# Optimization experiments

Measured on AMD Instinct MI355X. Metric: run time of the kernel, lower is better.

Reference implementation:

```python
import jax, jax.numpy as jnp
import numpy as np

D_MODEL = 1024
N_HEADS = 16
HEAD_DIM = D_MODEL // N_HEADS
N_SCALES = 11
_D4 = jnp.array([0.4829629131445341, 0.8365163037378079, 0.2241438680420134, -0.1294095225512604], dtype=jnp.float32)


def setup_inputs() -> dict:
    key = jax.random.key(0)
    ks = jax.random.split(key, 8)
    B, N, D = 8, 2048, D_MODEL
    s = 1.0 / np.sqrt(D)
    x = jax.random.normal(ks[0], (B, N, D), dtype=jnp.float32)
    qkv_w = jax.random.normal(ks[1], (3 * D, D), dtype=jnp.float32) * s
    qkv_b = jnp.zeros((3 * D,), dtype=jnp.float32)
    out_w = jax.random.normal(ks[2], (D, D), dtype=jnp.float32) * s
    out_b = jnp.zeros((D,), dtype=jnp.float32)
    gate_w = jax.random.normal(ks[3], (D, D), dtype=jnp.float32) * s
    gate_b = jnp.full((D,), 2.0, dtype=jnp.float32)  # nn.init.constant_(gate_proj.bias, 2.0)
    scale_gain = jax.random.normal(ks[4], (N_SCALES, N_HEADS), dtype=jnp.float32) * 0.1
    field_coupling = jnp.eye(N_HEADS, dtype=jnp.float32) + 0.01 * jax.random.normal(ks[5], (N_HEADS, N_HEADS), dtype=jnp.float32)
    return {"x": x, "qkv_w": qkv_w, "qkv_b": qkv_b, "out_w": out_w, "out_b": out_b,
            "gate_w": gate_w, "gate_b": gate_b, "scale_gain": scale_gain,
            "field_coupling": field_coupling}


def _causal_multiscale(x_c, scale_gain):
    # x_c: [B, C, N] with channel order (head-major, then head_dim)
    B, C, N = x_c.shape
    gains = jax.nn.softmax(scale_gain, axis=0)              # [S, H]
    gains_exp = jnp.repeat(gains, HEAD_DIM, axis=1)         # [S, C]
    out = jnp.zeros_like(x_c)
    for j in range(N_SCALES):
        d = 1 << j
        xp = jnp.pad(x_c, ((0, 0), (0, 0), (3 * d, 0)))     # causal left pad
        # depthwise dilated conv (cross-correlation, same D4 taps per channel)
        y = (_D4[0] * xp[:, :, 0 * d:0 * d + N]
             + _D4[1] * xp[:, :, 1 * d:1 * d + N]
             + _D4[2] * xp[:, :, 2 * d:2 * d + N]
             + _D4[3] * xp[:, :, 3 * d:3 * d + N])
        out = out + gains_exp[j][None, :, None] * y
    return out


def reference(x, qkv_w, qkv_b, out_w, out_b, gate_w, gate_b, scale_gain, field_coupling):
    B, N, D = x.shape
    H, HD = N_HEADS, HEAD_DIM
    qkv = x @ qkv_w.T + qkv_b                               # [B, N, 3D]
    q, k, v = jnp.split(qkv, 3, axis=-1)                    # q is unused (as in source)
    k = k.reshape(B, N, H, HD)
    v = v.reshape(B, N, H, HD)
    k_mag = jnp.linalg.norm(k, axis=-1, keepdims=True)      # [B, N, H, 1]
    field = v * k_mag                                       # [B, N, H, HD]
    # -> [B, C, N], C = H*HD, head-major channel layout
    x_c = jnp.transpose(field, (0, 2, 3, 1)).reshape(B, H * HD, N)
    out_c = _causal_multiscale(x_c, scale_gain)             # [B, C, N]
    field = out_c.reshape(B, H, HD, N)                      # [B, H, HD, N]
    coupling = jax.nn.softmax(field_coupling, axis=-1)      # [H, H]
    field = jnp.einsum('ij,bjdn->bidn', coupling, field)    # head coupling
    gathered = jnp.transpose(field, (0, 3, 1, 2)).reshape(B, N, D)
    gate = jax.nn.sigmoid(x @ gate_w.T + gate_b)
    return (gathered * gate) @ out_w.T + out_b
```

## Files before the change

kernel.cpp:

```cpp
#include <hip/hip_runtime.h>
#include <hip/hip_bf16.h>
#include <math.h>

#define BD 8
#define SN 2048
#define DM 1024
#define NH 16
#define HD 64
#define NS 11
#define NTAP 24
#define PAD 3072

typedef __attribute__((ext_vector_type(8))) short short8;
typedef __attribute__((ext_vector_type(4))) float floatx4;

constexpr int OFFS[NTAP] = {0, 1, 2, 3, 4, 6, 8, 12, 16, 24, 32, 48, 64, 96,
                            128, 192, 256, 384, 512, 768, 1024, 1536, 2048, 3072};

__device__ __forceinline__ void async_load16(const void* g, void* lds) {
    __builtin_amdgcn_global_load_lds(
        (const __attribute__((address_space(1))) void*)g,
        (__attribute__((address_space(3))) void*)lds,
        16, 0, 0);
}

__device__ __forceinline__ float bf2f(int v) {
    union { unsigned u; float f; } cv;
    cv.u = ((unsigned)v & 0xffffu) << 16;
    return cv.f;
}

__device__ __forceinline__ unsigned short f2bfbits(float x) {
    union { __hip_bfloat16 h; unsigned short u; } cv;
    cv.h = __float2bfloat16(x);
    return cv.u;
}

__global__ __launch_bounds__(256) void f2bf_kernel(const float* __restrict__ src,
                                                   __hip_bfloat16* __restrict__ dst,
                                                   int n4) {
    int i = blockIdx.x * 256 + threadIdx.x;
    if (i < n4) {
        const float4 v = reinterpret_cast<const float4*>(src)[i];
        union { __hip_bfloat16 h[4]; uint2 u; } cv;
        cv.h[0] = __float2bfloat16(v.x);
        cv.h[1] = __float2bfloat16(v.y);
        cv.h[2] = __float2bfloat16(v.z);
        cv.h[3] = __float2bfloat16(v.w);
        reinterpret_cast<uint2*>(dst)[i] = cv.u;
    }
}

__global__ void prep_kernel(const float* __restrict__ scale_gain,
                            const float* __restrict__ field_coupling,
                            const float* __restrict__ qkv_b,
                            const float* __restrict__ gate_b,
                            float* __restrict__ wtab,
                            float* __restrict__ cw,
                            float* __restrict__ biascat)
{
    const float D4[4] = {0.4829629131445341f, 0.8365163037378079f,
                         0.2241438680420134f, -0.1294095225512604f};
    int t = threadIdx.x;
    if (t < NH) {
        float g[NS];
        float m = -1e30f;
        for (int j = 0; j < NS; ++j) m = fmaxf(m, scale_gain[j * NH + t]);
        float s = 0.f;
        for (int j = 0; j < NS; ++j) { g[j] = expf(scale_gain[j * NH + t] - m); s += g[j]; }
        float inv = 1.f / s;
        for (int j = 0; j < NS; ++j) g[j] *= inv;
        for (int i = 0; i < NTAP; ++i) {
            float w = 0.f;
            for (int j = 0; j < NS; ++j)
                for (int tt = 0; tt < 4; ++tt)
                    if (((3 - tt) << j) == OFFS[i]) w += g[j] * D4[tt];
            wtab[i * NH + t] = w;
        }
    } else if (t < 2 * NH) {
        int r = t - NH;
        float m = -1e30f;
        for (int j = 0; j < NH; ++j) m = fmaxf(m, field_coupling[r * NH + j]);
        float e[NH]; float s = 0.f;
        for (int j = 0; j < NH; ++j) { e[j] = expf(field_coupling[r * NH + j] - m); s += e[j]; }
        float inv = 1.f / s;
        for (int j = 0; j < NH; ++j) cw[r * NH + j] = e[j] * inv;
    }
    for (int i = t; i < 2048; i += 256)
        biascat[i] = (i < 1024) ? qkv_b[1024 + i] : gate_b[i - 1024];
}

__global__ __launch_bounds__(256, 3) void gemm128_kernel(
    const __hip_bfloat16* __restrict__ A,
    const __hip_bfloat16* __restrict__ Bw,
    void* __restrict__ Cout,
    const float* __restrict__ bias,
    float* __restrict__ kmag,
    int M, int Nn, int K, int mode) {
    __shared__ short As[128 * 64];
    __shared__ short Bs[128 * 64];

    const int tid = threadIdx.x;
    const int m0 = blockIdx.y * 128;
    const int n0 = blockIdx.x * 128;
    const int wv = tid >> 6;
    const int ln = tid & 63;

    const int srow = ln >> 3;
    const int scc  = (ln & 7) ^ srow;
    size_t goffA[4], goffB[4];
    #pragma unroll
    for (int i = 0; i < 4; ++i) {
        const int row = wv * 32 + i * 8 + srow;
        goffA[i] = (size_t)(m0 + row) * K + scc * 8;
        goffB[i] = (size_t)(n0 + row) * K + scc * 8;
    }

    const int lrow = ln & 15, quad = ln >> 4;
    const int wm = (wv >> 1) * 64;
    const int wn = (wv & 1) * 64;
    int aaddr[4], baddr[4];
    #pragma unroll
    for (int t = 0; t < 4; ++t) {
        const int sw = (quad ^ (lrow & 7)) * 16;
        aaddr[t] = (wm + t * 16 + lrow) * 128 + sw;
        baddr[t] = (wn + t * 16 + lrow) * 128 + sw;
    }

    floatx4 acc[4][4];
    #pragma unroll
    for (int a = 0; a < 4; ++a)
        #pragma unroll
        for (int b = 0; b < 4; ++b) acc[a][b] = (floatx4){0.f, 0.f, 0.f, 0.f};

    for (int kt = 0; kt < K; kt += 64) {
        #pragma unroll
        for (int i = 0; i < 4; ++i) {
            async_load16(A + goffA[i] + kt, &As[(wv * 32 + i * 8) * 64]);
            async_load16(Bw + goffB[i] + kt, &Bs[(wv * 32 + i * 8) * 64]);
        }
        __syncthreads();
        #pragma unroll
        for (int h = 0; h < 2; ++h) {
            short8 a[4], b[4];
            #pragma unroll
            for (int t = 0; t < 4; ++t) {
                a[t] = *reinterpret_cast<const short8*>(
                           reinterpret_cast<const char*>(As) + (aaddr[t] ^ (h * 64)));
                b[t] = *reinterpret_cast<const short8*>(
                           reinterpret_cast<const char*>(Bs) + (baddr[t] ^ (h * 64)));
            }
            #pragma unroll
            for (int mt = 0; mt < 4; ++mt)
                #pragma unroll
                for (int nt = 0; nt < 4; ++nt)
                    acc[mt][nt] = __builtin_amdgcn_mfma_f32_16x16x32_bf16(
                        a[mt], b[nt], acc[mt][nt], 0, 0, 0);
        }
        __syncthreads();
    }

    if (mode == 2 && n0 < 1024) {
        const int h = (n0 + wn) >> 6;
        #pragma unroll
        for (int mt = 0; mt < 4; ++mt) {
            #pragma unroll
            for (int i = 0; i < 4; ++i) {
                float ss = 0.f;
                #pragma unroll
                for (int nt = 0; nt < 4; ++nt) {
                    const float v = acc[mt][nt][i] + bias[n0 + wn + nt * 16 + lrow];
                    ss += v * v;
                }
                ss += __shfl_xor(ss, 1);
                ss += __shfl_xor(ss, 2);
                ss += __shfl_xor(ss, 4);
                ss += __shfl_xor(ss, 8);
                if (lrow == 0) {
                    const int r = m0 + wm + mt * 16 + quad * 4 + i;
                    kmag[h * (BD * SN) + r] = sqrtf(ss);
                }
            }
        }
        return;
    }

    #pragma unroll
    for (int mt = 0; mt < 4; ++mt) {
        #pragma unroll
        for (int nt = 0; nt < 4; ++nt) {
            const int col = n0 + wn + nt * 16 + lrow;
            float bv = 0.f;
            if (bias && mode != 1) bv = bias[col];
            #pragma unroll
            for (int i = 0; i < 4; ++i) {
                const int row = m0 + wm + mt * 16 + quad * 4 + i;
                float val = acc[mt][nt][i] + bv;
                if (mode == 1 && bias) val += bias[row];
                if (mode == 0) {
                    ((float*)Cout)[(size_t)row * Nn + col] = val;
                } else if (mode == 1) {
                    ((__hip_bfloat16*)Cout)[(size_t)row * Nn + col] = __float2bfloat16(val);
                } else {
                    val = 1.f / (1.f + expf(-val));
                    ((__hip_bfloat16*)Cout)[(size_t)row * 1024 + (col - 1024)] =
                        __float2bfloat16(val);
                }
            }
        }
    }
}

__global__ __launch_bounds__(256) void wavelet_kernel(const __hip_bfloat16* __restrict__ fieldv,
                                                      const float* __restrict__ kmag,
                                                      const float* __restrict__ wtab,
                                                      __hip_bfloat16* __restrict__ wave) {
    const int bc = blockIdx.x;
    const int b = bc >> 10;
    const int c = bc & (DM - 1);
    const int h = c >> 6;
    __shared__ float row[PAD + SN];
    const int t = threadIdx.x;

    float w[NTAP];
    #pragma unroll
    for (int i = 0; i < NTAP; ++i) w[i] = wtab[i * NH + h];

    {
        float4* r4 = reinterpret_cast<float4*>(row);
        const float4 zv = {0.f, 0.f, 0.f, 0.f};
        #pragma unroll
        for (int i = 0; i < 3; ++i) r4[t + i * 256] = zv;
    }
    {
        const __hip_bfloat16* src = fieldv + (size_t)c * (BD * SN) + b * SN;
        const float* mag = kmag + (size_t)h * (BD * SN) + b * SN;
        const int i = t * 8;
        const short8 s = *reinterpret_cast<const short8*>(src + i);
        const float4 m0 = *reinterpret_cast<const float4*>(mag + i);
        const float4 m1 = *reinterpret_cast<const float4*>(mag + i + 4);
        float4 o0, o1;
        o0.x = bf2f(s[0]) * m0.x; o0.y = bf2f(s[1]) * m0.y;
        o0.z = bf2f(s[2]) * m0.z; o0.w = bf2f(s[3]) * m0.w;
        o1.x = bf2f(s[4]) * m1.x; o1.y = bf2f(s[5]) * m1.y;
        o1.z = bf2f(s[6]) * m1.z; o1.w = bf2f(s[7]) * m1.w;
        *reinterpret_cast<float4*>(&row[PAD + i]) = o0;
        *reinterpret_cast<float4*>(&row[PAD + i + 4]) = o1;
    }
    __syncthreads();

    __hip_bfloat16* dst = wave + (size_t)bc * SN;
    #pragma unroll
    for (int pass = 0; pass < 2; ++pass) {
        const int n = (pass * 256 + t) * 4;
        const float* bp = &row[PAD + n];
        const float4 qc = *reinterpret_cast<const float4*>(bp);
        const float4 qb = *reinterpret_cast<const float4*>(bp - 4);
        const float4 qa = *reinterpret_cast<const float4*>(bp - 8);
        float a0, a1, a2, a3;
        a0 = w[0] * qc.x; a1 = w[0] * qc.y; a2 = w[0] * qc.z; a3 = w[0] * qc.w;
        a0 += w[1] * qb.w; a1 += w[1] * qc.x; a2 += w[1] * qc.y; a3 += w[1] * qc.z;
        a0 += w[2] * qb.z; a1 += w[2] * qb.w; a2 += w[2] * qc.x; a3 += w[2] * qc.y;
        a0 += w[3] * qb.y; a1 += w[3] * qb.z; a2 += w[3] * qb.w; a3 += w[3] * qc.x;
        a0 += w[4] * qb.x; a1 += w[4] * qb.y; a2 += w[4] * qb.z; a3 += w[4] * qb.w;
        a0 += w[5] * qa.z; a1 += w[5] * qa.w; a2 += w[5] * qb.x; a3 += w[5] * qb.y;
        a0 += w[6] * qa.x; a1 += w[6] * qa.y; a2 += w[6] * qa.z; a3 += w[6] * qa.w;
        #pragma unroll
        for (int i = 7; i < NTAP; ++i) {
            const float4 q = *reinterpret_cast<const float4*>(bp - OFFS[i]);
            a0 += w[i] * q.x; a1 += w[i] * q.y; a2 += w[i] * q.z; a3 += w[i] * q.w;
        }
        union { __hip_bfloat16 hh[4]; uint2 u; } cv;
        cv.hh[0] = __float2bfloat16(a0); cv.hh[1] = __float2bfloat16(a1);
        cv.hh[2] = __float2bfloat16(a2); cv.hh[3] = __float2bfloat16(a3);
        *reinterpret_cast<uint2*>(dst + n) = cv.u;
    }
}

__global__ __launch_bounds__(256) void couplegate_kernel(
        const __hip_bfloat16* __restrict__ wave,
        const float* __restrict__ cw,
        const __hip_bfloat16* __restrict__ gate,
        __hip_bfloat16* __restrict__ Ag) {
    const int b = blockIdx.y;
    const int n0 = blockIdx.x * 32;
    __shared__ unsigned short U[33 * 1024];
    __shared__ float cwl[NH * NH];
    const int t = threadIdx.x;
    const int wv = t >> 6, ln = t & 63;

    #pragma unroll
    for (int p = 0; p < 16; ++p) {
        const int u = p * 256 + wv * 64 + ln;
        const int cch = u >> 2, qs = u & 3;
        const int qg = qs ^ (cch & 3);
        async_load16(wave + (size_t)(b * DM + cch) * SN + n0 + qg * 8,
                     (char*)U + (size_t)(p * 256 + wv * 64) * 16);
    }
    cwl[t] = cw[t];
    __syncthreads();

    const int nq = t & 7;
    const int d0 = t >> 3;
    const int d1 = 32 + d0;
    float v0[16][4], v1[16][4];
    #pragma unroll
    for (int hi = 0; hi < 16; ++hi) {
        #pragma unroll
        for (int q = 0; q < 4; ++q) {
            const int s0 = q ^ (d0 & 3);
            const int s1 = q ^ (d1 & 3);
            v0[hi][q] = bf2f(U[(hi * 64 + d0) * 32 + s0 * 8 + nq]);
            v1[hi][q] = bf2f(U[(hi * 64 + d1) * 32 + s1 * 8 + nq]);
        }
    }
    __syncthreads();

    #pragma unroll
    for (int ho = 0; ho < 16; ++ho) {
        float cwr[16];
        #pragma unroll
        for (int j = 0; j < 4; ++j) {
            const float4 c4 = *reinterpret_cast<const float4*>(&cwl[ho * 16 + j * 4]);
            cwr[j * 4 + 0] = c4.x; cwr[j * 4 + 1] = c4.y;
            cwr[j * 4 + 2] = c4.z; cwr[j * 4 + 3] = c4.w;
        }
        float a0[4] = {0.f, 0.f, 0.f, 0.f}, a1[4] = {0.f, 0.f, 0.f, 0.f};
        #pragma unroll
        for (int hi = 0; hi < 16; ++hi) {
            #pragma unroll
            for (int q = 0; q < 4; ++q) {
                a0[q] += cwr[hi] * v0[hi][q];
                a1[q] += cwr[hi] * v1[hi][q];
            }
        }
        #pragma unroll
        for (int q = 0; q < 4; ++q) {
            const int nloc = q * 8 + nq;
            U[nloc * 1032 + ho * 64 + d0] = f2bfbits(a0[q]);
            U[nloc * 1032 + ho * 64 + d1] = f2bfbits(a1[q]);
        }
    }
    __syncthreads();

    #pragma unroll
    for (int p = 0; p < 16; ++p) {
        const int idx = p * 256 + t;
        const int nloc = idx >> 7, cu = idx & 127;
        const short8 ov = *reinterpret_cast<const short8*>(&U[nloc * 1032 + cu * 8]);
        const size_t off = ((size_t)(b * SN + n0 + nloc)) * DM + cu * 8;
        const short8 gv = *reinterpret_cast<const short8*>(
            reinterpret_cast<const unsigned short*>(gate) + off);
        union { __hip_bfloat16 hh[8]; short8 s; } cv;
        #pragma unroll
        for (int j = 0; j < 8; ++j)
            cv.hh[j] = __float2bfloat16(bf2f(ov[j]) * bf2f(gv[j]));
        *reinterpret_cast<short8*>(reinterpret_cast<unsigned short*>(Ag) + off) = cv.s;
    }
}

extern "C" void kernel_launch(void* const* d_in, const int* in_sizes, int n_in,
                              void* d_out, int out_size, void* d_ws, size_t ws_size,
                              hipStream_t stream) {
    const float* x     = (const float*)d_in[0];
    const float* qkv_w = (const float*)d_in[1];
    const float* qkv_b = (const float*)d_in[2];
    const float* out_w = (const float*)d_in[3];
    const float* out_b = (const float*)d_in[4];
    const float* gate_w = (const float*)d_in[5];
    const float* gate_b = (const float*)d_in[6];
    const float* scale_gain = (const float*)d_in[7];
    const float* field_coupling = (const float*)d_in[8];

    char* ws = (char*)d_ws;
    const int M = BD * SN;

    __hip_bfloat16* x_bf    = (__hip_bfloat16*)(ws);
    __hip_bfloat16* wkg_bf  = (__hip_bfloat16*)(ws + 33554432);
    __hip_bfloat16* wv_bf   = (__hip_bfloat16*)(ws + 37748736);
    __hip_bfloat16* wo_bf   = (__hip_bfloat16*)(ws + 39845888);
    float* wtab             = (float*)(ws + 41943040);
    float* cwbuf            = (float*)(ws + 41944576);
    float* biascat          = (float*)(ws + 41945600);
    float* kmag             = (float*)(ws + 41953792);
    __hip_bfloat16* fieldv  = (__hip_bfloat16*)(ws + 43002368);
    __hip_bfloat16* gate_bf = (__hip_bfloat16*)(ws + 76556800);
    __hip_bfloat16* wave_bf = (__hip_bfloat16*)(ws + 110111232);
    __hip_bfloat16* Ag = x_bf;
    float* out = (float*)d_out;

    f2bf_kernel<<<(M * DM / 4 + 255) / 256, 256, 0, stream>>>(x, x_bf, M * DM / 4);
    f2bf_kernel<<<(DM * DM / 4 + 255) / 256, 256, 0, stream>>>(qkv_w + (size_t)DM * DM, wkg_bf, DM * DM / 4);
    f2bf_kernel<<<(DM * DM / 4 + 255) / 256, 256, 0, stream>>>(gate_w, wkg_bf + (size_t)DM * DM, DM * DM / 4);
    f2bf_kernel<<<(DM * DM / 4 + 255) / 256, 256, 0, stream>>>(qkv_w + (size_t)2 * DM * DM, wv_bf, DM * DM / 4);
    f2bf_kernel<<<(DM * DM / 4 + 255) / 256, 256, 0, stream>>>(out_w, wo_bf, DM * DM / 4);

    prep_kernel<<<1, 256, 0, stream>>>(scale_gain, field_coupling, qkv_b, gate_b,
                                       wtab, cwbuf, biascat);

    {
        dim3 grid(2 * DM / 128, M / 128);
        gemm128_kernel<<<grid, 256, 0, stream>>>(x_bf, wkg_bf, gate_bf, biascat, kmag,
                                                 M, 2 * DM, DM, 2);
    }
    {
        dim3 grid(M / 128, DM / 128);
        gemm128_kernel<<<grid, 256, 0, stream>>>(wv_bf, x_bf, fieldv, qkv_b + 2 * DM, nullptr,
                                                 DM, M, DM, 1);
    }
    wavelet_kernel<<<BD * DM, 256, 0, stream>>>(fieldv, kmag, wtab, wave_bf);
    {
        dim3 grid(SN / 32, BD);
        couplegate_kernel<<<grid, 256, 0, stream>>>(wave_bf, cwbuf, gate_bf, Ag);
    }
    {
        dim3 grid(DM / 128, M / 128);
        gemm128_kernel<<<grid, 256, 0, stream>>>(Ag, wo_bf, out, out_b, nullptr,
                                                 M, DM, DM, 0);
    }
}
```

Before: 400.0 us.

## Replace 128x128 GEMM with 256x256 tile, 8-wave, double-buffered pipelined kernel

```diff
diff --git a/kernel.cpp b/kernel.cpp
--- a/kernel.cpp
+++ b/kernel.cpp
@@ -90,86 +90,170 @@
         biascat[i] = (i < 1024) ? qkv_b[1024 + i] : gate_b[i - 1024];
 }
 
-__global__ __launch_bounds__(256, 3) void gemm128_kernel(
+
+#define PHASE_SYNC() do { \
+    __builtin_amdgcn_sched_barrier(0); \
+    __builtin_amdgcn_s_barrier(); \
+    asm volatile("s_waitcnt lgkmcnt(0)" ::: "memory"); \
+    __builtin_amdgcn_sched_barrier(0); \
+} while (0)
+
+#define PHASE_END() do { \
+    __builtin_amdgcn_sched_barrier(0); \
+    __builtin_amdgcn_s_barrier(); \
+} while (0)
+
+#define STAGE(GP, H, KT, LB) do { \
+    _Pragma("unroll") \
+    for (int jj = 0; jj < 2; ++jj) { \
+        const int grow_ = (H) * 128 + jj * 64 + srow; \
+        async_load16((GP) + (size_t)grow_ * K + (KT) + gk8, \
+                     &S[(LB) + ((H) * 128 + jj * 64 + wid8) * 64]); \
+    } \
+} while (0)
+
+#define READ_A(AV, P, MF0) do { \
+    _Pragma("unroll") \
+    for (int mm = 0; mm < 4; ++mm) { \
+        const int off_ = (P) * 32768 + abase + ((MF0) + mm) * 1024; \
+        AV[mm][0] = *reinterpret_cast<const short8*>(&S[off_ + sw0]); \
+        AV[mm][1] = *reinterpret_cast<const short8*>(&S[off_ + sw1]); \
+    } \
+} while (0)
+
+#define READ_B(P, NF0) do { \
+    _Pragma("unroll") \
+    for (int nn = 0; nn < 2; ++nn) { \
+        const int off_ = (P) * 32768 + bbase + ((NF0) + nn) * 1024; \
+        bfr[nn][0] = *reinterpret_cast<const short8*>(&S[off_ + sw0]); \
+        bfr[nn][1] = *reinterpret_cast<const short8*>(&S[off_ + sw1]); \
+    } \
+} while (0)
+
+#define MFMA_Q(AV, MF0, NF0) do { \
+    __builtin_amdgcn_s_setprio(1); \
+    _Pragma("unroll") \
+    for (int mm = 0; mm < 4; ++mm) \
+        _Pragma("unroll") \
+        for (int nn = 0; nn < 2; ++nn) \
+            _Pragma("unroll") \
+            for (int hh = 0; hh < 2; ++hh) \
+                acc[(MF0) + mm][(NF0) + nn] = __builtin_amdgcn_mfma_f32_16x16x32_bf16( \
+                    AV[mm][hh], bfr[nn][hh], acc[(MF0) + mm][(NF0) + nn], 0, 0, 0); \
+    __builtin_amdgcn_s_setprio(0); \
+} while (0)
+
+__global__ __launch_bounds__(512, 2) void gemm256_kernel(
     const __hip_bfloat16* __restrict__ A,
     const __hip_bfloat16* __restrict__ Bw,
     void* __restrict__ Cout,
     const float* __restrict__ bias,
     float* __restrict__ kmag,
     int M, int Nn, int K, int mode) {
-    __shared__ short As[128 * 64];
-    __shared__ short Bs[128 * 64];
+    __shared__ short S[65536];
 
     const int tid = threadIdx.x;
-    const int m0 = blockIdx.y * 128;
-    const int n0 = blockIdx.x * 128;
-    const int wv = tid >> 6;
-    const int ln = tid & 63;
-
-    const int srow = ln >> 3;
-    const int scc  = (ln & 7) ^ srow;
-    size_t goffA[4], goffB[4];
-    #pragma unroll
-    for (int i = 0; i < 4; ++i) {
-        const int row = wv * 32 + i * 8 + srow;
-        goffA[i] = (size_t)(m0 + row) * K + scc * 8;
-        goffB[i] = (size_t)(n0 + row) * K + scc * 8;
-    }
+    const int wid = tid >> 6;
+    const int ln  = tid & 63;
+    const int m0 = blockIdx.y * 256;
+    const int n0 = blockIdx.x * 256;
+
+    const int srow = tid >> 3;
+    const int gk8  = ((tid & 7) ^ (srow & 7)) * 8;
+    const int wid8 = wid * 8;
 
     const int lrow = ln & 15, quad = ln >> 4;
-    const int wm = (wv >> 1) * 64;
-    const int wn = (wv & 1) * 64;
-    int aaddr[4], baddr[4];
-    #pragma unroll
-    for (int t = 0; t < 4; ++t) {
-        const int sw = (quad ^ (lrow & 7)) * 16;
-        aaddr[t] = (wm + t * 16 + lrow) * 128 + sw;
-        baddr[t] = (wn + t * 16 + lrow) * 128 + sw;
-    }
-
-    floatx4 acc[4][4];
-    #pragma unroll
-    for (int a = 0; a < 4; ++a)
+    const int wm = (wid >> 2) * 128;
+    const int wn = (wid & 3) * 64;
+    const int sw0 = (quad ^ (lrow & 7)) * 8;
+    const int sw1 = ((4 + quad) ^ (lrow & 7)) * 8;
+    const int abase = (wm + lrow) * 64;
+    const int bbase = 16384 + (wn + lrow) * 64;
+
+    const __hip_bfloat16* Ab = A + (size_t)m0 * K;
+    const __hip_bfloat16* Bb = Bw + (size_t)n0 * K;
+
+    floatx4 acc[8][4];
+    #pragma unroll
+    for (int a = 0; a < 8; ++a)
         #pragma unroll
         for (int b = 0; b < 4; ++b) acc[a][b] = (floatx4){0.f, 0.f, 0.f, 0.f};
-
-    for (int kt = 0; kt < K; kt += 64) {
-        #pragma unroll
-        for (int i = 0; i < 4; ++i) {
-            async_load16(A + goffA[i] + kt, &As[(wv * 32 + i * 8) * 64]);
-            async_load16(Bw + goffB[i] + kt, &Bs[(wv * 32 + i * 8) * 64]);
-        }
-        __syncthreads();
-        #pragma unroll
-        for (int h = 0; h < 2; ++h) {
-            short8 a[4], b[4];
-            #pragma unroll
-            for (int t = 0; t < 4; ++t) {
-                a[t] = *reinterpret_cast<const short8*>(
-                           reinterpret_cast<const char*>(As) + (aaddr[t] ^ (h * 64)));
-                b[t] = *reinterpret_cast<const short8*>(
-                           reinterpret_cast<const char*>(Bs) + (baddr[t] ^ (h * 64)));
-            }
-            #pragma unroll
-            for (int mt = 0; mt < 4; ++mt)
-                #pragma unroll
-                for (int nt = 0; nt < 4; ++nt)
-                    acc[mt][nt] = __builtin_amdgcn_mfma_f32_16x16x32_bf16(
-                        a[mt], b[nt], acc[mt][nt], 0, 0, 0);
-        }
-        __syncthreads();
+    short8 a01[4][2], a23[4][2], bfr[2][2];
+
+    const int I = K >> 7;
+
+    STAGE(Ab, 0, 0, 0);
+    STAGE(Ab, 1, 0, 0);
+    STAGE(Bb, 0, 0, 16384);
+    STAGE(Bb, 1, 0, 16384);
+    STAGE(Ab, 0, 64, 32768);
+    STAGE(Ab, 1, 64, 32768);
+    asm volatile("s_waitcnt vmcnt(4)" ::: "memory");
+    __builtin_amdgcn_sched_barrier(0);
+    __builtin_amdgcn_s_barrier();
+
+    for (int i = 0; i < I; ++i) {
+        const int t1k = (2 * i + 1) * 64;
+        const int t2k = (2 * i + 2) * 64;
+        const int t3k = (2 * i + 3) * 64;
+        const bool notlast = (i < I - 1);
+
+        READ_A(a01, 0, 0); READ_B(0, 0);
+        STAGE(Bb, 0, t1k, 49152);
+        PHASE_SYNC();
+        MFMA_Q(a01, 0, 0);
+        PHASE_END();
+        READ_A(a23, 0, 4); READ_B(0, 2);
+        STAGE(Bb, 1, t1k, 49152);
+        PHASE_SYNC();
+        MFMA_Q(a01, 0, 2);
+        PHASE_END();
+        READ_B(0, 0);
+        if (notlast) STAGE(Ab, 0, t2k, 0);
+        PHASE_SYNC();
+        MFMA_Q(a23, 4, 0);
+        PHASE_END();
+        READ_B(0, 2);
+        if (notlast) STAGE(Ab, 1, t2k, 0);
+        PHASE_SYNC();
+        MFMA_Q(a23, 4, 2);
+        if (notlast) { asm volatile("s_waitcnt vmcnt(4)" ::: "memory"); }
+        else         { asm volatile("s_waitcnt vmcnt(0)" ::: "memory"); }
+        PHASE_END();
+
+        READ_A(a01, 1, 0); READ_B(1, 0);
+        if (notlast) STAGE(Bb, 0, t2k, 16384);
+        PHASE_SYNC();
+        MFMA_Q(a01, 0, 0);
+        PHASE_END();
+        READ_A(a23, 1, 4); READ_B(1, 2);
+        if (notlast) STAGE(Bb, 1, t2k, 16384);
+        PHASE_SYNC();
+        MFMA_Q(a01, 0, 2);
+        PHASE_END();
+        READ_B(1, 0);
+        if (notlast) STAGE(Ab, 0, t3k, 32768);
+        PHASE_SYNC();
+        MFMA_Q(a23, 4, 0);
+        PHASE_END();
+        READ_B(1, 2);
+        if (notlast) STAGE(Ab, 1, t3k, 32768);
+        PHASE_SYNC();
+        MFMA_Q(a23, 4, 2);
+        if (notlast) { asm volatile("s_waitcnt vmcnt(4)" ::: "memory"); }
+        PHASE_END();
     }
 
     if (mode == 2 && n0 < 1024) {
         const int h = (n0 + wn) >> 6;
         #pragma unroll
-        for (int mt = 0; mt < 4; ++mt) {
+        for (int mf = 0; mf < 8; ++mf) {
             #pragma unroll
-            for (int i = 0; i < 4; ++i) {
+            for (int i4 = 0; i4 < 4; ++i4) {
                 float ss = 0.f;
                 #pragma unroll
-                for (int nt = 0; nt < 4; ++nt) {
-                    const float v = acc[mt][nt][i] + bias[n0 + wn + nt * 16 + lrow];
+                for (int nf = 0; nf < 4; ++nf) {
+                    const float v = acc[mf][nf][i4] + bias[n0 + wn + nf * 16 + lrow];
                     ss += v * v;
                 }
                 ss += __shfl_xor(ss, 1);
@@ -177,7 +261,7 @@
                 ss += __shfl_xor(ss, 4);
                 ss += __shfl_xor(ss, 8);
                 if (lrow == 0) {
-                    const int r = m0 + wm + mt * 16 + quad * 4 + i;
+                    const int r = m0 + wm + mf * 16 + quad * 4 + i4;
                     kmag[h * (BD * SN) + r] = sqrtf(ss);
                 }
             }
@@ -186,16 +270,16 @@
     }
 
     #pragma unroll
-    for (int mt = 0; mt < 4; ++mt) {
-        #pragma unroll
-        for (int nt = 0; nt < 4; ++nt) {
-            const int col = n0 + wn + nt * 16 + lrow;
+    for (int mf = 0; mf < 8; ++mf) {
+        #pragma unroll
+        for (int nf = 0; nf < 4; ++nf) {
+            const int col = n0 + wn + nf * 16 + lrow;
             float bv = 0.f;
             if (bias && mode != 1) bv = bias[col];
             #pragma unroll
-            for (int i = 0; i < 4; ++i) {
-                const int row = m0 + wm + mt * 16 + quad * 4 + i;
-                float val = acc[mt][nt][i] + bv;
+            for (int i4 = 0; i4 < 4; ++i4) {
+                const int row = m0 + wm + mf * 16 + quad * 4 + i4;
+                float val = acc[mf][nf][i4] + bv;
                 if (mode == 1 && bias) val += bias[row];
                 if (mode == 0) {
                     ((float*)Cout)[(size_t)row * Nn + col] = val;
@@ -210,6 +294,13 @@
         }
     }
 }
+
+#undef PHASE_SYNC
+#undef PHASE_END
+#undef STAGE
+#undef READ_A
+#undef READ_B
+#undef MFMA_Q
 
 __global__ __launch_bounds__(256) void wavelet_kernel(const __hip_bfloat16* __restrict__ fieldv,
                                                       const float* __restrict__ kmag,
@@ -399,13 +490,13 @@
                                        wtab, cwbuf, biascat);
 
     {
-        dim3 grid(2 * DM / 128, M / 128);
-        gemm128_kernel<<<grid, 256, 0, stream>>>(x_bf, wkg_bf, gate_bf, biascat, kmag,
+        dim3 grid(2 * DM / 256, M / 256);
+        gemm256_kernel<<<grid, 512, 0, stream>>>(x_bf, wkg_bf, gate_bf, biascat, kmag,
                                                  M, 2 * DM, DM, 2);
     }
     {
-        dim3 grid(M / 128, DM / 128);
-        gemm128_kernel<<<grid, 256, 0, stream>>>(wv_bf, x_bf, fieldv, qkv_b + 2 * DM, nullptr,
+        dim3 grid(M / 256, DM / 256);
+        gemm256_kernel<<<grid, 512, 0, stream>>>(wv_bf, x_bf, fieldv, qkv_b + 2 * DM, nullptr,
                                                  DM, M, DM, 1);
     }
     wavelet_kernel<<<BD * DM, 256, 0, stream>>>(fieldv, kmag, wtab, wave_bf);
@@ -414,8 +505,8 @@
         couplegate_kernel<<<grid, 256, 0, stream>>>(wave_bf, cwbuf, gate_bf, Ag);
     }
     {
-        dim3 grid(DM / 128, M / 128);
-        gemm128_kernel<<<grid, 256, 0, stream>>>(Ag, wo_bf, out, out_b, nullptr,
+        dim3 grid(DM / 256, M / 256);
+        gemm256_kernel<<<grid, 512, 0, stream>>>(Ag, wo_bf, out, out_b, nullptr,
                                                  M, DM, DM, 0);
     }
 }
```

Result: slower. 443.8 us (+10.9%).
